# Optimization experiments

Hardware: AMD Instinct MI355X
Metric: run time of the kernel (lower is better)

## Reference

```python
import jax, jax.numpy as jnp
import numpy as np

EPS = 1e-5
NUM_SUBSET = 3

def conv1x1(x, w, b):
    # x: (N,C,T,V), w: (O,C), b: (O,)
    return jnp.einsum('nctv,oc->notv', x, w) + b[None, :, None, None]

def batchnorm(x, w, b):
    m = x.mean(axis=(0, 2, 3), keepdims=True)
    v = x.var(axis=(0, 2, 3), keepdims=True)
    return (x - m) * jax.lax.rsqrt(v + EPS) * w[None, :, None, None] + b[None, :, None, None]

def setup_inputs() -> dict:
    key = jax.random.key(0)
    ks = jax.random.split(key, 16)
    N, C, T, V, R, O, S = 32, 64, 256, 25, 8, 64, NUM_SUBSET
    sc = 0.05
    return {
        'x1': jax.random.normal(ks[0], (N, C, T, V), jnp.float32),
        'x2': jax.random.normal(ks[1], (N, C, T, V), jnp.float32),
        'PA': jax.random.normal(ks[2], (S, V, V), jnp.float32) * sc,
        'alpha': jnp.zeros((1,), jnp.float32),
        'c1w': jax.random.normal(ks[3], (S, R, C), jnp.float32) * sc,
        'c1b': jnp.zeros((S, R), jnp.float32),
        'c2w': jax.random.normal(ks[4], (S, R, C), jnp.float32) * sc,
        'c2b': jnp.zeros((S, R), jnp.float32),
        'c3w': jax.random.normal(ks[5], (S, O, C), jnp.float32) * sc,
        'c3b': jnp.zeros((S, O), jnp.float32),
        'c4w': jax.random.normal(ks[6], (S, O, C), jnp.float32) * sc,
        'c4b': jnp.zeros((S, O), jnp.float32),
        'c5w': jax.random.normal(ks[7], (S, O, R), jnp.float32) * sc,
        'c5b': jnp.zeros((S, O), jnp.float32),
        'c6w': jax.random.normal(ks[8], (S, O, R), jnp.float32) * sc,
        'c6b': jnp.zeros((S, O), jnp.float32),
        'bn1_w': jax.random.uniform(ks[9], (O,), jnp.float32),
        'bn1_b': jnp.zeros((O,), jnp.float32),
        'bn2_w': jax.random.uniform(ks[10], (O,), jnp.float32),
        'bn2_b': jnp.zeros((O,), jnp.float32),
    }

def reference(x1, x2, PA, alpha, c1w, c1b, c2w, c2b, c3w, c3b, c4w, c4b,
              c5w, c5b, c6w, c6b, bn1_w, bn1_b, bn2_w, bn2_b):
    y1 = y2 = None
    for i in range(NUM_SUBSET):
        r1 = conv1x1(x1, c1w[i], c1b[i]).mean(axis=2)  # (N,R,V)
        r2 = conv1x1(x2, c2w[i], c2b[i]).mean(axis=2)  # (N,R,V)
        x3 = conv1x1(x1, c3w[i], c3b[i])               # (N,O,T,V)
        x4 = conv1x1(x2, c4w[i], c4b[i])               # (N,O,T,V)
        rel = jnp.tanh(r1[:, :, :, None] - r2[:, :, None, :])  # (N,R,V,V)
        # NOTE: source passes self.alpha (scalar param) into the A2 slot,
        # so the `alpha` multiplier on conv5 defaults to 1.
        a1 = jnp.einsum('nruv,or->nouv', rel, c5w[i]) + c5b[i][None, :, None, None]
        a1 = a1 + PA[i][None, None, :, :]
        a2 = jnp.einsum('nruv,or->nouv', rel, c6w[i]) + c6b[i][None, :, None, None] + alpha
        z1 = jnp.einsum('ncuv,nctv->nctu', a1, x3)
        z2 = jnp.einsum('ncuv,nctv->nctu', a2, x4)
        y1 = z1 if y1 is None else y1 + z1
        y2 = z2 if y2 is None else y2 + z2
    # in_channels == out_channels -> residual down is identity
    y1 = jax.nn.relu(batchnorm(y1, bn1_w, bn1_b) + x1)
    y2 = jax.nn.relu(batchnorm(y2, bn2_w, bn2_b) + x2)
    return (y1, y2)
```

## Files before the change

kernel.cpp:

```cpp
#include <hip/hip_runtime.h>

typedef float  f32x4  __attribute__((ext_vector_type(4)));
typedef short  bf16x8 __attribute__((ext_vector_type(8)));
typedef short  s16x4  __attribute__((ext_vector_type(4)));

__device__ __forceinline__ unsigned short f2bf(float f) {
    unsigned int u = __float_as_uint(f);
    unsigned int r = (u + 0x7FFFu + ((u >> 16) & 1u)) >> 16;
    return (unsigned short)r;
}
__device__ __forceinline__ float bf2f(unsigned short h) {
    return __uint_as_float(((unsigned int)h) << 16);
}

__global__ __launch_bounds__(256) void kT_transpose(
    const float* __restrict__ x1, const float* __restrict__ x2,
    float* __restrict__ xm, unsigned short* __restrict__ xT)
{
    const int tc = blockIdx.x, n = blockIdx.y, p = blockIdx.z;
    const float* __restrict__ x = p ? x2 : x1;
    __shared__ unsigned short tile[64 * 225];
    const int tid = threadIdx.x;

    const size_t xb = (size_t)n * 409600 + (size_t)tc * 200;
    for (int k = 0; k < 13; k++) {
        const int idx = tid + k * 256;
        if (idx < 3200) {
            const int c = idx / 50, l = idx % 50;
            const f32x4 v = *(const f32x4*)(x + xb + (size_t)c * 6400 + l * 4);
            const int base = c * 225 + l * 4;
            tile[base + 0] = f2bf(v[0]);
            tile[base + 1] = f2bf(v[1]);
            tile[base + 2] = f2bf(v[2]);
            tile[base + 3] = f2bf(v[3]);
        }
    }
    __syncthreads();

    for (int k = 0; k < 7; k++) {
        const int idx = tid + k * 256;
        if (idx < 1600) {
            const int c = idx / 25, v = idx % 25;
            float s = 0.f;
            #pragma unroll
            for (int t = 0; t < 8; t++) s += bf2f(tile[c * 225 + t * 25 + v]);
            atomicAdd(&xm[((size_t)(p * 32 + n) * 64 + c) * 25 + v],
                      s * (1.0f / 256.0f));
        }
    }

    for (int k = 0; k < 7; k++) {
        const int idx = tid + k * 256;
        if (idx < 1600) {
            const int c8 = idx & 7, pos = idx >> 3;
            bf16x8 o;
            #pragma unroll
            for (int j = 0; j < 8; j++)
                o[j] = (short)tile[(c8 * 8 + j) * 225 + pos];
            *(bf16x8*)(xT + (((size_t)(p * 32 + n) * 6400 + tc * 200 + pos) * 64
                             + c8 * 8)) = o;
        }
    }
}

__global__ void k2_adj(const float* __restrict__ xm,
                       const float* __restrict__ PA, const float* __restrict__ alpha,
                       const float* __restrict__ c1w, const float* __restrict__ c1b,
                       const float* __restrict__ c2w, const float* __restrict__ c2b,
                       const float* __restrict__ c5w, const float* __restrict__ c5b,
                       const float* __restrict__ c6w, const float* __restrict__ c6b,
                       unsigned short* __restrict__ aw,
                       const float* __restrict__ c3w, const float* __restrict__ c4w,
                       unsigned short* __restrict__ awW)
{
    const int b = blockIdx.x;
    const int tid = threadIdx.x;

    if (b >= 192) {
        const int pi = b - 192;
        const int p = pi / 3, i = pi % 3;
        const int cg = tid >> 6, lane = tid & 63, q = lane >> 4, m = lane & 15;
        const float* w3 = p ? c4w : c3w;
        const float* wr = w3 + (size_t)(i * 64 + cg * 16 + m) * 64 + q * 8;
        const f32x4 w00 = *(const f32x4*)(wr);
        const f32x4 w01 = *(const f32x4*)(wr + 4);
        const f32x4 w10 = *(const f32x4*)(wr + 32);
        const f32x4 w11 = *(const f32x4*)(wr + 36);
        bf16x8 af0, af1;
        #pragma unroll
        for (int k = 0; k < 4; k++) {
            af0[k] = (short)f2bf(w00[k]); af0[k + 4] = (short)f2bf(w01[k]);
            af1[k] = (short)f2bf(w10[k]); af1[k + 4] = (short)f2bf(w11[k]);
        }
        unsigned short* o = awW + ((size_t)(pi * 4 + cg) * 64 + lane) * 16;
        *(bf16x8*)(o)     = af0;
        *(bf16x8*)(o + 8) = af1;
        return;
    }

    const int i = b >> 6;
    const int n = (b >> 1) & 31;
    const int pp = b & 1;
    __shared__ float xml[3200];
    __shared__ float rl[400];
    __shared__ float rel[5000];

    for (int idx = tid; idx < 3200; idx += 256) {
        const int p_ = idx / 1600, rest = idx % 1600;
        xml[idx] = xm[(size_t)(p_ * 32 + n) * 1600 + rest];
    }
    __syncthreads();

    for (int idx = tid; idx < 400; idx += 256) {
        const int which = idx / 200;
        const int rr = (idx % 200) / 25;
        const int v = idx % 25;
        const float* wv = (which ? c2w : c1w) + (i * 8 + rr) * 64;
        const float* xp = xml + which * 1600;
        float s = (which ? c2b : c1b)[i * 8 + rr];
        for (int c = 0; c < 64; c++) s += wv[c] * xp[c * 25 + v];
        rl[idx] = s;
    }
    __syncthreads();

    for (int idx = tid; idx < 5000; idx += 256) {
        const int r_ = idx / 625;
        const int rem = idx - r_ * 625;
        const int u = rem / 25;
        const int v = rem - u * 25;
        rel[idx] = tanhf(rl[r_ * 25 + u] - rl[200 + r_ * 25 + v]);
    }
    __syncthreads();

    const float al = alpha[0];
    {
        const int p_ = pp;
        const float* w5 = p_ ? c6w : c5w;
        const float* b5 = p_ ? c6b : c5b;
        for (int idx = tid; idx < 8192; idx += 256) {
            const int c = idx >> 7;
            const int ut = (idx >> 6) & 1;
            const int lane = idx & 63;
            const int u = ut * 16 + (lane & 15);
            const int qd = lane >> 4;
            bf16x8 outv;
            if (u < 25) {
                float wrow[8];
                #pragma unroll
                for (int r = 0; r < 8; r++) wrow[r] = w5[(i * 64 + c) * 8 + r];
                const float bias = b5[i * 64 + c];
                #pragma unroll
                for (int j = 0; j < 8; j++) {
                    const int v = qd * 8 + j;
                    float s = 0.f;
                    if (v < 25) {
                        s = bias + (p_ ? al : PA[i * 625 + u * 25 + v]);
                        #pragma unroll
                        for (int r = 0; r < 8; r++) s += rel[r * 625 + u * 25 + v] * wrow[r];
                    }
                    outv[j] = (short)f2bf(s);
                }
            } else {
                #pragma unroll
                for (int j = 0; j < 8; j++) outv[j] = 0;
            }
            *(bf16x8*)(aw + ((size_t)((p_ * 3 + i) * 32 + n) * 64 + c) * 1024
                          + ut * 512 + lane * 8) = outv;
        }
    }
}

__global__ __launch_bounds__(256, 3) void kF_main(
    const unsigned short* __restrict__ xT,
    const float* __restrict__ c3b, const float* __restrict__ c4b,
    const unsigned short* __restrict__ awW,
    const unsigned short* __restrict__ aw,
    unsigned short* __restrict__ z,
    float* __restrict__ ppart)
{
    const int flat = blockIdx.x;
    const int lidx = flat >> 3;
    const int grp  = (flat & 7) * 8 + (lidx >> 6);
    const int within = lidx & 63;
    const int tc = within & 15, cg = within >> 4;
    const int n = grp & 31, p = grp >> 5;

    __shared__ unsigned short X3s[2][16 * 512];
    const int tid = threadIdx.x, w = tid >> 6, lane = tid & 63;
    const int q = lane >> 4, m = lane & 15;

    {
        int* xi = (int*)&X3s[0][0];
        #pragma unroll
        for (int k = 0; k < 32; k++) xi[tid + k * 256] = 0;
    }

    const float* __restrict__ b3 = p ? c4b : c3b;
    const size_t xTb = ((size_t)(p * 32 + n) * 6400 + (size_t)tc * 400) * 64;

    bf16x8 xr0[7], xr1[7];
    #pragma unroll
    for (int k = 0; k < 7; k++) {
        const int g = w + 4 * k;
        if (g < 25) {
            const unsigned short* xp = xT + xTb + (size_t)(g * 16 + m) * 64 + q * 8;
            xr0[k] = *(const bf16x8*)(xp);
            xr1[k] = *(const bf16x8*)(xp + 32);
        }
    }

    f32x4 acc[4][2];
    #pragma unroll
    for (int a = 0; a < 4; a++) {
        acc[a][0] = (f32x4){0.f, 0.f, 0.f, 0.f};
        acc[a][1] = (f32x4){0.f, 0.f, 0.f, 0.f};
    }

    __syncthreads();

    for (int i = 0; i < 3; i++) {
        bf16x8 B0[4], B1[4];
        #pragma unroll
        for (int cl4 = 0; cl4 < 4; cl4++) {
            const int c = cg * 16 + w * 4 + cl4;
            const unsigned short* ab =
                aw + ((size_t)((p * 3 + i) * 32 + n) * 64 + c) * 1024 + lane * 8;
            B0[cl4] = *(const bf16x8*)(ab);
            B1[cl4] = *(const bf16x8*)(ab + 512);
        }

        const unsigned short* wp =
            awW + ((size_t)((p * 3 + i) * 4 + cg) * 64 + lane) * 16;
        const bf16x8 af0 = *(const bf16x8*)(wp);
        const bf16x8 af1 = *(const bf16x8*)(wp + 8);
        float bb[4];
        #pragma unroll
        for (int r = 0; r < 4; r++) bb[r] = b3[i * 64 + cg * 16 + q * 4 + r];

        unsigned short* Xb = &X3s[i & 1][0];
        #pragma unroll
        for (int k = 0; k < 7; k++) {
            const int g = w + 4 * k;
            if (g < 25) {
                f32x4 d = (f32x4){0.f, 0.f, 0.f, 0.f};
                d = __builtin_amdgcn_mfma_f32_16x16x32_bf16(af0, xr0[k], d, 0, 0, 0);
                d = __builtin_amdgcn_mfma_f32_16x16x32_bf16(af1, xr1[k], d, 0, 0, 0);
                const int pos = g * 16 + m;
                const int t = pos / 25, v = pos - t * 25;
                #pragma unroll
                for (int r = 0; r < 4; r++)
                    Xb[(q * 4 + r) * 512 + t * 32 + v] = f2bf(d[r] + bb[r]);
            }
        }
        __syncthreads();

        #pragma unroll
        for (int cl4 = 0; cl4 < 4; cl4++) {
            const int cl = w * 4 + cl4;
            const bf16x8 A = *(const bf16x8*)(Xb + cl * 512 + m * 32 + q * 8);
            acc[cl4][0] = __builtin_amdgcn_mfma_f32_16x16x32_bf16(A, B0[cl4], acc[cl4][0], 0, 0, 0);
            acc[cl4][1] = __builtin_amdgcn_mfma_f32_16x16x32_bf16(A, B1[cl4], acc[cl4][1], 0, 0, 0);
        }
    }
    __syncthreads();

    unsigned short* stg = &X3s[0][0];
    #pragma unroll
    for (int cl4 = 0; cl4 < 4; cl4++) {
        float sum = 0.f, ssq = 0.f;
        #pragma unroll
        for (int r = 0; r < 4; r++) {
            const float v0 = acc[cl4][0][r];
            sum += v0; ssq += v0 * v0;
        }
        if (m < 9) {
            #pragma unroll
            for (int r = 0; r < 4; r++) {
                const float v1 = acc[cl4][1][r];
                sum += v1; ssq += v1 * v1;
            }
        }
        #pragma unroll
        for (int off = 32; off > 0; off >>= 1) {
            sum += __shfl_xor(sum, off, 64);
            ssq += __shfl_xor(ssq, off, 64);
        }
        const int c = cg * 16 + w * 4 + cl4;
        if (lane == 0) {
            float* pp = ppart + ((size_t)(p * 64 + c) * 512 + n * 16 + tc) * 2;
            pp[0] = sum; pp[1] = ssq;
        }
        #pragma unroll
        for (int ut = 0; ut < 2; ut++) {
            if (ut == 0 || m < 9) {
                #pragma unroll
                for (int r = 0; r < 4; r++)
                    stg[w * 1600 + cl4 * 400 + (q * 4 + r) * 25 + ut * 16 + m] =
                        f2bf(acc[cl4][ut][r]);
            }
        }
    }
    for (int rd = 0; rd < 4; rd++) {
        const int idx = rd * 64 + lane;
        if (idx < 200) {
            const int cl4 = idx / 50, oct = idx % 50;
            const bf16x8 vz = *(const bf16x8*)(stg + w * 1600 + cl4 * 400 + oct * 8);
            const int c = cg * 16 + w * 4 + cl4;
            *(bf16x8*)(z + ((size_t)((p * 32 + n) * 64 + c)) * 6400
                         + tc * 400 + oct * 8) = vz;
        }
    }
}

__global__ void k4_finalize(const float* __restrict__ ppart,
                            const float* __restrict__ bn1w, const float* __restrict__ bn1b,
                            const float* __restrict__ bn2w, const float* __restrict__ bn2b,
                            float* __restrict__ ss)
{
    const int b = blockIdx.x;
    const int t = threadIdx.x;
    const float* base = ppart + (size_t)b * 1024;
    float s = 0.f, qs = 0.f;
    #pragma unroll
    for (int k = 0; k < 8; k++) {
        const int idx = t + 64 * k;
        s  += base[idx * 2];
        qs += base[idx * 2 + 1];
    }
    #pragma unroll
    for (int off = 32; off > 0; off >>= 1) {
        s  += __shfl_xor(s,  off, 64);
        qs += __shfl_xor(qs, off, 64);
    }
    if (t == 0) {
        const int p = b >> 6, c = b & 63;
        const float cnt = 204800.f;
        const float mean = s / cnt;
        const float var  = qs / cnt - mean * mean;
        const float gw = p ? bn2w[c] : bn1w[c];
        const float gb = p ? bn2b[c] : bn1b[c];
        const float scale = gw * rsqrtf(var + 1e-5f);
        ss[b * 2]     = scale;
        ss[b * 2 + 1] = gb - mean * scale;
    }
}

__global__ __launch_bounds__(256) void k5_apply(
    const float* __restrict__ x1, const float* __restrict__ x2,
    const unsigned short* __restrict__ z, const float* __restrict__ ss,
    float* __restrict__ out)
{
    const unsigned int g = blockIdx.x * 256u + threadIdx.x;
    const unsigned int e = g * 4u;
    const int p = (e >= 13107200u) ? 1 : 0;
    const unsigned int c = (e / 6400u) & 63u;
    const float* xsrc = p ? x2 : x1;
    const f32x4 xv = *(const f32x4*)(xsrc + (e - (unsigned int)p * 13107200u));
    const s16x4 zv = *(const s16x4*)(const void*)(z + e);
    const float scale = ss[(p * 64 + c) * 2];
    const float shift = ss[(p * 64 + c) * 2 + 1];
    f32x4 o;
    #pragma unroll
    for (int k = 0; k < 4; k++) {
        const float zf = bf2f((unsigned short)zv[k]);
        const float y = zf * scale + shift + xv[k];
        o[k] = y > 0.f ? y : 0.f;
    }
    *(f32x4*)(out + e) = o;
}

extern "C" void kernel_launch(void* const* d_in, const int* in_sizes, int n_in,
                              void* d_out, int out_size, void* d_ws, size_t ws_size,
                              hipStream_t stream)
{
    (void)in_sizes; (void)n_in; (void)out_size; (void)ws_size;
    const float* x1   = (const float*)d_in[0];
    const float* x2   = (const float*)d_in[1];
    const float* PA   = (const float*)d_in[2];
    const float* alp  = (const float*)d_in[3];
    const float* c1w  = (const float*)d_in[4];
    const float* c1b  = (const float*)d_in[5];
    const float* c2w  = (const float*)d_in[6];
    const float* c2b  = (const float*)d_in[7];
    const float* c3w  = (const float*)d_in[8];
    const float* c3b  = (const float*)d_in[9];
    const float* c4w  = (const float*)d_in[10];
    const float* c4b  = (const float*)d_in[11];
    const float* c5w  = (const float*)d_in[12];
    const float* c5b  = (const float*)d_in[13];
    const float* c6w  = (const float*)d_in[14];
    const float* c6b  = (const float*)d_in[15];
    const float* bn1w = (const float*)d_in[16];
    const float* bn1b = (const float*)d_in[17];
    const float* bn2w = (const float*)d_in[18];
    const float* bn2b = (const float*)d_in[19];

    char* ws = (char*)d_ws;
    float*          xm    = (float*)(ws + 0);
    unsigned short* aw    = (unsigned short*)(ws + 409600);
    unsigned short* xT    = (unsigned short*)(ws + 25575424);
    unsigned short* zbuf  = (unsigned short*)(ws + 78004224);
    float*          ppart = (float*)(ws + 130433024);
    float*          ss    = (float*)(ws + 130957312);
    unsigned short* awW   = (unsigned short*)(ws + 130958336);

    hipMemsetAsync(xm, 0, 409600, stream);

    kT_transpose<<<dim3(32, 32, 2), 256, 0, stream>>>(x1, x2, xm, xT);
    k2_adj<<<198, 256, 0, stream>>>(xm, PA, alp, c1w, c1b, c2w, c2b,
                                    c5w, c5b, c6w, c6b, aw, c3w, c4w, awW);
    kF_main<<<dim3(4096), 256, 0, stream>>>(xT, c3b, c4b, awW, aw,
                                            zbuf, ppart);
    k4_finalize<<<128, 64, 0, stream>>>(ppart, bn1w, bn1b, bn2w, bn2b, ss);
    k5_apply<<<25600, 256, 0, stream>>>(x1, x2, zbuf, ss, (float*)d_out);
}
```

Baseline: 373.8 us.

## Replace atomic mean reduction with partials; single-buffer main LDS for higher occupancy

The transpose kernel now writes per-time-chunk partial means into a scratch area aliased onto the z buffer, and the adjacency kernel sums those partials. This removes the global atomics and the memset. The main kernel drops its double-buffered shared tile to a single buffer with a sync after each subset, and its launch bound goes from 3 to 4 waves per SIMD to raise occupancy. The transpose converts floats to bf16 in pairs with the packed library intrinsic and pads its tile stride. The cost is an extra barrier per subset iteration and more register pressure under the tighter launch bound.

```diff
diff --git a/kernel.cpp b/kernel.cpp
--- a/kernel.cpp
+++ b/kernel.cpp
@@ -1,10 +1,19 @@
 #include <hip/hip_runtime.h>
+#include <hip/hip_bf16.h>
 
 typedef float  f32x4  __attribute__((ext_vector_type(4)));
 typedef short  bf16x8 __attribute__((ext_vector_type(8)));
 typedef short  s16x4  __attribute__((ext_vector_type(4)));
 
 __device__ __forceinline__ unsigned short f2bf(float f) {
+    __hip_bfloat16 h = __float2bfloat16(f);
+    return *reinterpret_cast<unsigned short*>(&h);
+}
+__device__ __forceinline__ unsigned int f2bf2(float a, float b) {
+    __hip_bfloat162 h = __float22bfloat162_rn(make_float2(a, b));
+    return *reinterpret_cast<unsigned int*>(&h);
+}
+__device__ __forceinline__ unsigned short f2bf_bit(float f) {
     unsigned int u = __float_as_uint(f);
     unsigned int r = (u + 0x7FFFu + ((u >> 16) & 1u)) >> 16;
     return (unsigned short)r;
@@ -15,11 +24,11 @@
 
 __global__ __launch_bounds__(256) void kT_transpose(
     const float* __restrict__ x1, const float* __restrict__ x2,
-    float* __restrict__ xm, unsigned short* __restrict__ xT)
+    float* __restrict__ xmp, unsigned short* __restrict__ xT)
 {
     const int tc = blockIdx.x, n = blockIdx.y, p = blockIdx.z;
     const float* __restrict__ x = p ? x2 : x1;
-    __shared__ unsigned short tile[64 * 225];
+    __shared__ unsigned short tile[64 * 226];
     const int tid = threadIdx.x;
 
     const size_t xb = (size_t)n * 409600 + (size_t)tc * 200;
@@ -28,11 +37,9 @@
         if (idx < 3200) {
             const int c = idx / 50, l = idx % 50;
             const f32x4 v = *(const f32x4*)(x + xb + (size_t)c * 6400 + l * 4);
-            const int base = c * 225 + l * 4;
-            tile[base + 0] = f2bf(v[0]);
-            tile[base + 1] = f2bf(v[1]);
-            tile[base + 2] = f2bf(v[2]);
-            tile[base + 3] = f2bf(v[3]);
+            unsigned int* dst = (unsigned int*)&tile[c * 226 + l * 4];
+            dst[0] = f2bf2(v[0], v[1]);
+            dst[1] = f2bf2(v[2], v[3]);
         }
     }
     __syncthreads();
@@ -43,9 +50,9 @@
             const int c = idx / 25, v = idx % 25;
             float s = 0.f;
             #pragma unroll
-            for (int t = 0; t < 8; t++) s += bf2f(tile[c * 225 + t * 25 + v]);
-            atomicAdd(&xm[((size_t)(p * 32 + n) * 64 + c) * 25 + v],
-                      s * (1.0f / 256.0f));
+            for (int t = 0; t < 8; t++) s += bf2f(tile[c * 226 + t * 25 + v]);
+            xmp[((size_t)((p * 32 + n) * 32 + tc)) * 1600 + idx] =
+                s * (1.0f / 256.0f);
         }
     }
 
@@ -56,14 +63,14 @@
             bf16x8 o;
             #pragma unroll
             for (int j = 0; j < 8; j++)
-                o[j] = (short)tile[(c8 * 8 + j) * 225 + pos];
+                o[j] = (short)tile[(c8 * 8 + j) * 226 + pos];
             *(bf16x8*)(xT + (((size_t)(p * 32 + n) * 6400 + tc * 200 + pos) * 64
                              + c8 * 8)) = o;
         }
     }
 }
 
-__global__ void k2_adj(const float* __restrict__ xm,
+__global__ void k2_adj(const float* __restrict__ xmp,
                        const float* __restrict__ PA, const float* __restrict__ alpha,
                        const float* __restrict__ c1w, const float* __restrict__ c1b,
                        const float* __restrict__ c2w, const float* __restrict__ c2b,
@@ -105,9 +112,13 @@
     __shared__ float rl[400];
     __shared__ float rel[5000];
 
-    for (int idx = tid; idx < 3200; idx += 256) {
-        const int p_ = idx / 1600, rest = idx % 1600;
-        xml[idx] = xm[(size_t)(p_ * 32 + n) * 1600 + rest];
+    for (int idx = tid; idx < 800; idx += 256) {
+        const int p_ = idx / 400, r4 = (idx % 400) * 4;
+        f32x4 s = (f32x4){0.f, 0.f, 0.f, 0.f};
+        #pragma unroll 4
+        for (int tcc = 0; tcc < 32; tcc++)
+            s += *(const f32x4*)(xmp + ((size_t)((p_ * 32 + n) * 32 + tcc)) * 1600 + r4);
+        *(f32x4*)(xml + p_ * 1600 + r4) = s;
     }
     __syncthreads();
 
@@ -170,7 +181,7 @@
     }
 }
 
-__global__ __launch_bounds__(256, 3) void kF_main(
+__global__ __launch_bounds__(256, 4) void kF_main(
     const unsigned short* __restrict__ xT,
     const float* __restrict__ c3b, const float* __restrict__ c4b,
     const unsigned short* __restrict__ awW,
@@ -185,14 +196,14 @@
     const int tc = within & 15, cg = within >> 4;
     const int n = grp & 31, p = grp >> 5;
 
-    __shared__ unsigned short X3s[2][16 * 512];
+    __shared__ unsigned short X3s[16 * 512];
     const int tid = threadIdx.x, w = tid >> 6, lane = tid & 63;
     const int q = lane >> 4, m = lane & 15;
 
     {
-        int* xi = (int*)&X3s[0][0];
-        #pragma unroll
-        for (int k = 0; k < 32; k++) xi[tid + k * 256] = 0;
+        int* xi = (int*)X3s;
+        #pragma unroll
+        for (int k = 0; k < 16; k++) xi[tid + k * 256] = 0;
     }
 
     const float* __restrict__ b3 = p ? c4b : c3b;
@@ -237,7 +248,6 @@
         #pragma unroll
         for (int r = 0; r < 4; r++) bb[r] = b3[i * 64 + cg * 16 + q * 4 + r];
 
-        unsigned short* Xb = &X3s[i & 1][0];
         #pragma unroll
         for (int k = 0; k < 7; k++) {
             const int g = w + 4 * k;
@@ -249,7 +259,7 @@
                 const int t = pos / 25, v = pos - t * 25;
                 #pragma unroll
                 for (int r = 0; r < 4; r++)
-                    Xb[(q * 4 + r) * 512 + t * 32 + v] = f2bf(d[r] + bb[r]);
+                    X3s[(q * 4 + r) * 512 + t * 32 + v] = f2bf_bit(d[r] + bb[r]);
             }
         }
         __syncthreads();
@@ -257,14 +267,14 @@
         #pragma unroll
         for (int cl4 = 0; cl4 < 4; cl4++) {
             const int cl = w * 4 + cl4;
-            const bf16x8 A = *(const bf16x8*)(Xb + cl * 512 + m * 32 + q * 8);
+            const bf16x8 A = *(const bf16x8*)(X3s + cl * 512 + m * 32 + q * 8);
             acc[cl4][0] = __builtin_amdgcn_mfma_f32_16x16x32_bf16(A, B0[cl4], acc[cl4][0], 0, 0, 0);
             acc[cl4][1] = __builtin_amdgcn_mfma_f32_16x16x32_bf16(A, B1[cl4], acc[cl4][1], 0, 0, 0);
         }
-    }
-    __syncthreads();
-
-    unsigned short* stg = &X3s[0][0];
+        __syncthreads();
+    }
+
+    unsigned short* stg = X3s;
     #pragma unroll
     for (int cl4 = 0; cl4 < 4; cl4++) {
         float sum = 0.f, ssq = 0.f;
@@ -296,7 +306,7 @@
                 #pragma unroll
                 for (int r = 0; r < 4; r++)
                     stg[w * 1600 + cl4 * 400 + (q * 4 + r) * 25 + ut * 16 + m] =
-                        f2bf(acc[cl4][ut][r]);
+                        f2bf_bit(acc[cl4][ut][r]);
             }
         }
     }
@@ -396,18 +406,16 @@
     const float* bn2b = (const float*)d_in[19];
 
     char* ws = (char*)d_ws;
-    float*          xm    = (float*)(ws + 0);
-    unsigned short* aw    = (unsigned short*)(ws + 409600);
-    unsigned short* xT    = (unsigned short*)(ws + 25575424);
-    unsigned short* zbuf  = (unsigned short*)(ws + 78004224);
-    float*          ppart = (float*)(ws + 130433024);
-    float*          ss    = (float*)(ws + 130957312);
-    unsigned short* awW   = (unsigned short*)(ws + 130958336);
-
-    hipMemsetAsync(xm, 0, 409600, stream);
-
-    kT_transpose<<<dim3(32, 32, 2), 256, 0, stream>>>(x1, x2, xm, xT);
-    k2_adj<<<198, 256, 0, stream>>>(xm, PA, alp, c1w, c1b, c2w, c2b,
+    unsigned short* aw    = (unsigned short*)(ws + 0);
+    unsigned short* xT    = (unsigned short*)(ws + 25165824);
+    unsigned short* zbuf  = (unsigned short*)(ws + 77594624);
+    float*          ppart = (float*)(ws + 130023424);
+    float*          ss    = (float*)(ws + 130547712);
+    unsigned short* awW   = (unsigned short*)(ws + 130548736);
+    float*          xmp   = (float*)zbuf;
+
+    kT_transpose<<<dim3(32, 32, 2), 256, 0, stream>>>(x1, x2, xmp, xT);
+    k2_adj<<<198, 256, 0, stream>>>(xmp, PA, alp, c1w, c1b, c2w, c2b,
                                     c5w, c5b, c6w, c6b, aw, c3w, c4w, awW);
     kF_main<<<dim3(4096), 256, 0, stream>>>(xT, c3b, c4b, awW, aw,
                                             zbuf, ppart);
```

Measured after the change: 445.2 us. +19.1%, slower.
